# Optimization experiments

Hardware: AMD Instinct MI355X
Metric: run time of the kernel (lower is better)

Reference implementation:

```python
import jax, jax.numpy as jnp
import numpy as np


def cosine_noise_schedule(t):
    # legacy mode: 1 - cos(t/1.008 * pi/2)^2
    return 1.0 - jnp.cos(t / 1.008 * jnp.pi / 2.0) ** 2


def setup_inputs() -> dict:
    key = jax.random.key(0)
    k1, k2, k3 = jax.random.split(key, 3)
    x = jax.random.normal(k1, (256, 3, 32, 32), dtype=jnp.float32)
    images = jax.random.normal(k2, (50000, 3, 32, 32), dtype=jnp.float32)
    t = jax.random.uniform(k3, (1,), dtype=jnp.float32)
    return {"t": t, "x": x, "images": images}


def reference(t, x, images):
    # Exact ideal score: softmax over dataset of Gaussian kernel weights.
    # The original streams dataset batches with an online-softmax running max;
    # with uniform batch sizes that is mathematically a global softmax over N:
    #   score = -(x - at * E_p[y]) / bt^2,  p_j = softmax(-||x - at*y_j||^2 / (2 bt^2))
    sched = cosine_noise_schedule(t)          # [1]
    bt = jnp.sqrt(sched)                      # [1]
    at = jnp.sqrt(1.0 - sched)                # [1]
    b, c, h, w = x.shape
    n = images.shape[0]
    xf = x.reshape(b, -1)                     # [b, chw]
    yf = images.reshape(n, -1)                # [n, chw]
    # ||x - at*y||^2 = ||x||^2 + at^2 ||y||^2 - 2 at x.y  (GEMM-dominant)
    x2 = jnp.sum(xf * xf, axis=1)             # [b]
    y2 = jnp.sum(yf * yf, axis=1)             # [n]
    cross = xf @ yf.T                         # [b, n]
    d2 = x2[:, None] + (at ** 2) * y2[None, :] - 2.0 * at * cross  # [b, n]
    logits = -d2 / (2.0 * bt ** 2)            # [b, n]
    p = jax.nn.softmax(logits, axis=1)        # [b, n], stable (max-subtracted)
    ybar = (p @ yf).reshape(b, c, h, w)       # softmax-weighted dataset mean
    return -(x - at * ybar) / (bt ** 2)
```

## Files before the change

kernel.cpp:

```cpp
#include <hip/hip_runtime.h>

typedef float    f32x4  __attribute__((ext_vector_type(4)));
typedef float    f32x16 __attribute__((ext_vector_type(16)));
typedef _Float16 f16x4  __attribute__((ext_vector_type(4)));
typedef _Float16 f16x8  __attribute__((ext_vector_type(8)));

#define N_IMG 50000
#define NPAD  50176
#define BROWS 256
#define CHW   3072
#define BK    64
#define BM    128
#define BN    128
#define EHS   50176
#define KCHUNK 3136
#define NSPLIT 16

__device__ __forceinline__ void glds16(const void* g, void* l) {
    __builtin_amdgcn_global_load_lds(
        (const __attribute__((address_space(1))) void*)g,
        (__attribute__((address_space(3))) void*)l, 16, 0, 0);
}

__global__ void k_scalars(const float* __restrict__ t, float* __restrict__ sc) {
    if (threadIdx.x == 0) {
        double tv  = (double)t[0];
        double ang = tv * (1.5707963267948966 / 1.008);
        double c   = cos(ang);
        double at  = c;
        double bt2 = 1.0 - c * c;
        sc[0] = (float)at;
        sc[1] = (float)bt2;
        sc[2] = (float)(at / bt2);
        sc[3] = (float)(at * at * 0.5 / bt2);
        sc[4] = (float)(1.0 / bt2);
    }
}

__global__ void k_xprep(const float* __restrict__ x, _Float16* __restrict__ xh) {
    int idx = blockIdx.x * 256 + threadIdx.x;
    f32x4 v = ((const f32x4*)x)[idx];
    f16x4 h;
    h[0] = (_Float16)v[0]; h[1] = (_Float16)v[1];
    h[2] = (_Float16)v[2]; h[3] = (_Float16)v[3];
    ((f16x4*)xh)[idx] = h;
}

__global__ void k_prep(const float* __restrict__ img, _Float16* __restrict__ imgh,
                       float* __restrict__ y2) {
    int row = blockIdx.x, tid = threadIdx.x;
    f16x4* dst = (f16x4*)(imgh + (size_t)row * CHW);
    if (row >= N_IMG) {
        f16x4 z = {(_Float16)0.f, (_Float16)0.f, (_Float16)0.f, (_Float16)0.f};
        #pragma unroll
        for (int i = 0; i < 3; i++) dst[tid + i * 256] = z;
        return;
    }
    const f32x4* src = (const f32x4*)(img + (size_t)row * CHW);
    float s = 0.f;
    #pragma unroll
    for (int i = 0; i < 3; i++) {
        f32x4 v = src[tid + i * 256];
        s += v[0]*v[0] + v[1]*v[1] + v[2]*v[2] + v[3]*v[3];
        f16x4 h;
        h[0] = (_Float16)v[0]; h[1] = (_Float16)v[1];
        h[2] = (_Float16)v[2]; h[3] = (_Float16)v[3];
        dst[tid + i * 256] = h;
    }
    for (int o = 32; o > 0; o >>= 1) s += __shfl_down(s, o);
    __shared__ float wsum[4];
    if ((tid & 63) == 0) wsum[tid >> 6] = s;
    __syncthreads();
    if (tid == 0) y2[row] = (wsum[0] + wsum[1]) + (wsum[2] + wsum[3]);
}

__global__ __launch_bounds__(256, 3) void k_gemm1(
        const _Float16* __restrict__ xh, const _Float16* __restrict__ imgh,
        const float* __restrict__ y2g, const float* __restrict__ sc,
        float* __restrict__ logits) {
    __shared__ _Float16 Alds[BM * BK];
    __shared__ _Float16 Blds[BN * BK];

    const int tid = threadIdx.x;
    const int wid = tid >> 6, lane = tid & 63;
    const int flat = blockIdx.x;
    const int xcd = flat & 7, loc = flat >> 3;
    const int m0 = (loc & 1) * BM;
    const int n0 = (xcd * 49 + (loc >> 1)) * BN;

    const _Float16* gA[4]; const _Float16* gB[4];
    _Float16* lA[4]; _Float16* lB[4];
    #pragma unroll
    for (int j = 0; j < 4; j++) {
        int seg = wid * 4 + j;
        int row = seg * 8 + (lane >> 3);
        int off = (((lane & 7) ^ (row & 7)) << 3);
        gA[j] = xh + (size_t)(m0 + row) * CHW + off;
        int rb = n0 + row; if (rb > N_IMG - 1) rb = N_IMG - 1;
        gB[j] = imgh + (size_t)rb * CHW + off;
        lA[j] = Alds + seg * 512;
        lB[j] = Blds + seg * 512;
    }

    const int wm = wid >> 1, wn = wid & 1;
    const int rm = wm * 64, cn = wn * 64;
    const int lr = lane & 31, hi = lane >> 5;
    const int xm = (lr & 7) << 4;
    const char* Ab = (const char*)Alds;
    const char* Bb = (const char*)Blds;
    const int ar0 = (rm + lr) * 128,      ar1 = (rm + 32 + lr) * 128;
    const int br0 = (cn + lr) * 128,      br1 = (cn + 32 + lr) * 128;
    const int kof = hi * 16;

    f32x16 acc[2][2];
    #pragma unroll
    for (int mi = 0; mi < 2; mi++)
        #pragma unroll
        for (int ni = 0; ni < 2; ni++)
            #pragma unroll
            for (int r = 0; r < 16; r++) acc[mi][ni][r] = 0.f;

    for (int it = 0; it < CHW / BK; ++it) {
        if (it) __syncthreads();
        #pragma unroll
        for (int j = 0; j < 4; j++) glds16(gA[j] + it * BK, lA[j]);
        #pragma unroll
        for (int j = 0; j < 4; j++) glds16(gB[j] + it * BK, lB[j]);
        __syncthreads();
        #pragma unroll
        for (int ks = 0; ks < 4; ++ks) {
            int off = (ks * 32 + kof) ^ xm;
            f16x8 a0 = *(const f16x8*)(Ab + ar0 + off);
            f16x8 a1 = *(const f16x8*)(Ab + ar1 + off);
            f16x8 b0 = *(const f16x8*)(Bb + br0 + off);
            f16x8 b1 = *(const f16x8*)(Bb + br1 + off);
            acc[0][0] = __builtin_amdgcn_mfma_f32_32x32x16_f16(a0, b0, acc[0][0], 0, 0, 0);
            acc[0][1] = __builtin_amdgcn_mfma_f32_32x32x16_f16(a0, b1, acc[0][1], 0, 0, 0);
            acc[1][0] = __builtin_amdgcn_mfma_f32_32x32x16_f16(a1, b0, acc[1][0], 0, 0, 0);
            acc[1][1] = __builtin_amdgcn_mfma_f32_32x32x16_f16(a1, b1, acc[1][1], 0, 0, 0);
        }
    }

    const float c_cross = sc[2], c_y2 = sc[3];
    #pragma unroll
    for (int mi = 0; mi < 2; mi++)
        #pragma unroll
        for (int ni = 0; ni < 2; ni++) {
            int col = n0 + cn + ni * 32 + lr;
            if (col >= N_IMG) continue;
            float y2v = y2g[col];
            f32x16 v = acc[mi][ni];
            #pragma unroll
            for (int r = 0; r < 16; r++) {
                int row = m0 + rm + mi * 32 + (r & 3) + 8 * (r >> 2) + 4 * hi;
                logits[(size_t)row * N_IMG + col] = c_cross * v[r] - c_y2 * y2v;
            }
        }
}

__global__ void k_softmax(const float* __restrict__ logits, _Float16* __restrict__ eh,
                          float* __restrict__ rowsum) {
    int row = blockIdx.x, tid = threadIdx.x;
    const f32x4* lr = (const f32x4*)(logits + (size_t)row * N_IMG);
    _Float16* erow = eh + (size_t)row * EHS;
    f16x4* er = (f16x4*)erow;
    __shared__ float wred[4];

    if (tid < EHS - N_IMG) erow[N_IMG + tid] = (_Float16)0.f;

    float m = -3.0e38f;
    for (int i = tid; i < N_IMG / 4; i += 256) {
        f32x4 v = lr[i];
        m = fmaxf(m, fmaxf(fmaxf(v[0], v[1]), fmaxf(v[2], v[3])));
    }
    for (int o = 32; o > 0; o >>= 1) m = fmaxf(m, __shfl_down(m, o));
    if ((tid & 63) == 0) wred[tid >> 6] = m;
    __syncthreads();
    m = fmaxf(fmaxf(wred[0], wred[1]), fmaxf(wred[2], wred[3]));
    __syncthreads();

    float s = 0.f;
    for (int i = tid; i < N_IMG / 4; i += 256) {
        f32x4 v = lr[i];
        float e0 = __expf(v[0] - m), e1 = __expf(v[1] - m);
        float e2 = __expf(v[2] - m), e3 = __expf(v[3] - m);
        s += (e0 + e1) + (e2 + e3);
        f16x4 h;
        h[0] = (_Float16)e0; h[1] = (_Float16)e1;
        h[2] = (_Float16)e2; h[3] = (_Float16)e3;
        er[i] = h;
    }
    for (int o = 32; o > 0; o >>= 1) s += __shfl_down(s, o);
    if ((tid & 63) == 0) wred[tid >> 6] = s;
    __syncthreads();
    if (tid == 0) rowsum[row] = (wred[0] + wred[1]) + (wred[2] + wred[3]);
}

__global__ __launch_bounds__(256, 2) void k_gemm2(
        const _Float16* __restrict__ eh, const _Float16* __restrict__ imgh,
        float* __restrict__ partial) {
    __shared__ _Float16 Alds[2][BM * BK];
    __shared__ _Float16 Blds[BN * BK];
    __shared__ _Float16 Tmp[BK * BN];

    const int tid = threadIdx.x;
    const int wid = tid >> 6, lane = tid & 63;
    const int flat = blockIdx.x;
    const int xcd = flat & 7, loc = flat >> 3;
    const int ck  = xcd * 2 + (loc >= 48 ? 1 : 0);
    const int rem = loc - (loc >= 48 ? 48 : 0);
    const int m0 = (rem & 1) * BM;
    const int d0 = (rem >> 1) * BN;
    const int kbase = ck * KCHUNK;

    const _Float16* gA[4]; int lAo[4];
    const _Float16* gB[4]; _Float16* lB[4];
    #pragma unroll
    for (int j = 0; j < 4; j++) {
        int seg = wid * 4 + j;
        int row = seg * 8 + (lane >> 3);
        int off = (((lane & 7) ^ (row & 7)) << 3);
        gA[j] = eh + (size_t)(m0 + row) * EHS + kbase + off;
        lAo[j] = seg * 512;
        gB[j] = imgh + (size_t)(kbase + seg * 4 + (lane >> 4)) * CHW + d0 + (lane & 15) * 8;
        lB[j] = Tmp + seg * 512;
    }

    const int wm = wid >> 1, wn = wid & 1;
    const int rm = wm * 64, cn = wn * 64;
    const int lr = lane & 31, hi = lane >> 5;
    const int xm = (lr & 7) << 4;
    const int ar0 = (rm + lr) * 128, ar1 = (rm + 32 + lr) * 128;
    const int br0 = (cn + lr) * 128, br1 = (cn + 32 + lr) * 128;
    const int kof = hi * 16;

    f32x16 acc[2][2];
    #pragma unroll
    for (int mi = 0; mi < 2; mi++)
        #pragma unroll
        for (int ni = 0; ni < 2; ni++)
            #pragma unroll
            for (int r = 0; r < 16; r++) acc[mi][ni][r] = 0.f;

    #pragma unroll
    for (int j = 0; j < 4; j++) glds16(gA[j], (_Float16*)Alds[0] + lAo[j]);
    #pragma unroll
    for (int j = 0; j < 4; j++) glds16(gB[j], lB[j]);

    int c = 0;
    for (int it = 0; it < KCHUNK / BK; ++it) {
        __syncthreads();
        #pragma unroll
        for (int tt = 0; tt < 4; tt++) {
            int gid = tid + tt * 256;
            int d = gid & 127, oct = gid >> 7;
            f16x8 w;
            #pragma unroll
            for (int j = 0; j < 8; j++) w[j] = Tmp[(oct * 8 + j) * 128 + d];
            *(f16x8*)((char*)Blds + d * 128 + ((oct ^ (d & 7)) << 4)) = w;
        }
        __syncthreads();
        if (it + 1 < KCHUNK / BK) {
            #pragma unroll
            for (int j = 0; j < 4; j++)
                glds16(gA[j] + (it + 1) * BK, (_Float16*)Alds[c ^ 1] + lAo[j]);
            #pragma unroll
            for (int j = 0; j < 4; j++)
                glds16(gB[j] + (size_t)(it + 1) * BK * CHW, lB[j]);
        }
        const char* Ab = (const char*)Alds[c];
        const char* Bb = (const char*)Blds;
        #pragma unroll
        for (int ks = 0; ks < 4; ++ks) {
            int off = (ks * 32 + kof) ^ xm;
            f16x8 a0 = *(const f16x8*)(Ab + ar0 + off);
            f16x8 a1 = *(const f16x8*)(Ab + ar1 + off);
            f16x8 b0 = *(const f16x8*)(Bb + br0 + off);
            f16x8 b1 = *(const f16x8*)(Bb + br1 + off);
            acc[0][0] = __builtin_amdgcn_mfma_f32_32x32x16_f16(a0, b0, acc[0][0], 0, 0, 0);
            acc[0][1] = __builtin_amdgcn_mfma_f32_32x32x16_f16(a0, b1, acc[0][1], 0, 0, 0);
            acc[1][0] = __builtin_amdgcn_mfma_f32_32x32x16_f16(a1, b0, acc[1][0], 0, 0, 0);
            acc[1][1] = __builtin_amdgcn_mfma_f32_32x32x16_f16(a1, b1, acc[1][1], 0, 0, 0);
        }
        c ^= 1;
    }

    float* pp = partial + (size_t)ck * BROWS * CHW;
    #pragma unroll
    for (int mi = 0; mi < 2; mi++)
        #pragma unroll
        for (int ni = 0; ni < 2; ni++) {
            int dcol = d0 + cn + ni * 32 + lr;
            f32x16 v = acc[mi][ni];
            #pragma unroll
            for (int r = 0; r < 16; r++) {
                int row = m0 + rm + mi * 32 + (r & 3) + 8 * (r >> 2) + 4 * hi;
                pp[(size_t)row * CHW + dcol] = v[r];
            }
        }
}

__global__ void k_final(const float* __restrict__ partial, const float* __restrict__ x,
                        const float* __restrict__ rowsum, const float* __restrict__ sc,
                        float* __restrict__ out) {
    int idx = blockIdx.x * 256 + threadIdx.x;
    int row = idx / (CHW / 4);
    float at = sc[0], invbt2 = sc[4];
    float scale = at * invbt2 / rowsum[row];
    const f32x4* p4 = (const f32x4*)partial;
    f32x4 s = p4[idx];
    #pragma unroll
    for (int c = 1; c < NSPLIT; c++) s = s + p4[(size_t)c * (BROWS * CHW / 4) + idx];
    f32x4 xv = ((const f32x4*)x)[idx];
    f32x4 o;
    #pragma unroll
    for (int j = 0; j < 4; j++) o[j] = s[j] * scale - xv[j] * invbt2;
    ((f32x4*)out)[idx] = o;
}

extern "C" void kernel_launch(void* const* d_in, const int* in_sizes, int n_in,
                              void* d_out, int out_size, void* d_ws, size_t ws_size,
                              hipStream_t stream) {
    const float* t   = (const float*)d_in[0];
    const float* x   = (const float*)d_in[1];
    const float* img = (const float*)d_in[2];
    float* out = (float*)d_out;
    char* ws = (char*)d_ws;

    float*    sc     = (float*)(ws + 0);
    float*    rowsum = (float*)(ws + 256);
    float*    y2     = (float*)(ws + 4096);
    _Float16* xh     = (_Float16*)(ws + 212992);
    _Float16* imgh   = (_Float16*)(ws + 2097152);
    _Float16* eh     = (_Float16*)(ws + 310378496);
    float*    logits = (float*)(ws + 336068608);
    float*    partial = logits;

    k_scalars<<<1, 64, 0, stream>>>(t, sc);
    k_xprep<<<(BROWS * CHW / 4) / 256, 256, 0, stream>>>(x, xh);
    k_prep<<<NPAD, 256, 0, stream>>>(img, imgh, y2);
    k_gemm1<<<784, 256, 0, stream>>>(xh, imgh, y2, sc, logits);
    k_softmax<<<256, 256, 0, stream>>>(logits, eh, rowsum);
    k_gemm2<<<768, 256, 0, stream>>>(eh, imgh, partial);
    k_final<<<(BROWS * CHW / 4) / 256, 256, 0, stream>>>(partial, x, rowsum, sc, out);
}
```

Before: 524.5 us.

## Drop A double buffering to fit three blocks per CU and vectorize B transpose

Result: faster. 481.5 us (-8.2%).

```diff
diff --git a/kernel.cpp b/kernel.cpp
--- a/kernel.cpp
+++ b/kernel.cpp
@@ -196,10 +196,10 @@
     if (tid == 0) rowsum[row] = (wred[0] + wred[1]) + (wred[2] + wred[3]);
 }
 
-__global__ __launch_bounds__(256, 2) void k_gemm2(
+__global__ __launch_bounds__(256, 3) void k_gemm2(
         const _Float16* __restrict__ eh, const _Float16* __restrict__ imgh,
         float* __restrict__ partial) {
-    __shared__ _Float16 Alds[2][BM * BK];
+    __shared__ _Float16 Alds[BM * BK];
     __shared__ _Float16 Blds[BN * BK];
     __shared__ _Float16 Tmp[BK * BN];
 
@@ -213,7 +213,7 @@
     const int d0 = (rem >> 1) * BN;
     const int kbase = ck * KCHUNK;
 
-    const _Float16* gA[4]; int lAo[4];
+    const _Float16* gA[4]; _Float16* lA[4];
     const _Float16* gB[4]; _Float16* lB[4];
     #pragma unroll
     for (int j = 0; j < 4; j++) {
@@ -221,10 +221,13 @@
         int row = seg * 8 + (lane >> 3);
         int off = (((lane & 7) ^ (row & 7)) << 3);
         gA[j] = eh + (size_t)(m0 + row) * EHS + kbase + off;
-        lAo[j] = seg * 512;
+        lA[j] = Alds + seg * 512;
         gB[j] = imgh + (size_t)(kbase + seg * 4 + (lane >> 4)) * CHW + d0 + (lane & 15) * 8;
         lB[j] = Tmp + seg * 512;
     }
+
+    const int q   = tid & 31;
+    const int oct = tid >> 5;
 
     const int wm = wid >> 1, wn = wid & 1;
     const int rm = wm * 64, cn = wn * 64;
@@ -242,33 +245,31 @@
             #pragma unroll
             for (int r = 0; r < 16; r++) acc[mi][ni][r] = 0.f;
 
-    #pragma unroll
-    for (int j = 0; j < 4; j++) glds16(gA[j], (_Float16*)Alds[0] + lAo[j]);
-    #pragma unroll
-    for (int j = 0; j < 4; j++) glds16(gB[j], lB[j]);
-
-    int c = 0;
     for (int it = 0; it < KCHUNK / BK; ++it) {
         __syncthreads();
         #pragma unroll
-        for (int tt = 0; tt < 4; tt++) {
-            int gid = tid + tt * 256;
-            int d = gid & 127, oct = gid >> 7;
-            f16x8 w;
-            #pragma unroll
-            for (int j = 0; j < 8; j++) w[j] = Tmp[(oct * 8 + j) * 128 + d];
-            *(f16x8*)((char*)Blds + d * 128 + ((oct ^ (d & 7)) << 4)) = w;
-        }
+        for (int j = 0; j < 4; j++) glds16(gA[j] + it * BK, lA[j]);
+        #pragma unroll
+        for (int j = 0; j < 4; j++) glds16(gB[j] + (size_t)it * BK * CHW, lB[j]);
         __syncthreads();
-        if (it + 1 < KCHUNK / BK) {
-            #pragma unroll
-            for (int j = 0; j < 4; j++)
-                glds16(gA[j] + (it + 1) * BK, (_Float16*)Alds[c ^ 1] + lAo[j]);
-            #pragma unroll
-            for (int j = 0; j < 4; j++)
-                glds16(gB[j] + (size_t)(it + 1) * BK * CHW, lB[j]);
-        }
-        const char* Ab = (const char*)Alds[c];
+
+        {
+            f16x4 r[8];
+            #pragma unroll
+            for (int j = 0; j < 8; j++)
+                r[j] = *(const f16x4*)&Tmp[(oct * 8 + j) * 128 + q * 4];
+            #pragma unroll
+            for (int dd = 0; dd < 4; dd++) {
+                f16x8 w;
+                #pragma unroll
+                for (int j = 0; j < 8; j++) w[j] = r[j][dd];
+                int d = q * 4 + dd;
+                *(f16x8*)((char*)Blds + d * 128 + ((oct ^ (d & 7)) << 4)) = w;
+            }
+        }
+        __syncthreads();
+
+        const char* Ab = (const char*)Alds;
         const char* Bb = (const char*)Blds;
         #pragma unroll
         for (int ks = 0; ks < 4; ++ks) {
@@ -282,7 +283,6 @@
             acc[1][0] = __builtin_amdgcn_mfma_f32_32x32x16_f16(a1, b0, acc[1][0], 0, 0, 0);
             acc[1][1] = __builtin_amdgcn_mfma_f32_32x32x16_f16(a1, b1, acc[1][1], 0, 0, 0);
         }
-        c ^= 1;
     }
 
     float* pp = partial + (size_t)ck * BROWS * CHW;
```
